# Performance work log

Hardware: AMD Instinct MI355X
Metric: run time of the kernel (lower is better)

The kernel has to match this reference:

```python
import jax, jax.numpy as jnp
import numpy as np

B = 8192      # batch_size
D = 1024      # d_model
E = 8         # num_domains
OUT = 2       # binary fake/real logits


def setup_inputs() -> dict:
    key = jax.random.key(0)
    k_feat, k_ids, k_w1, k_b1, k_w2, k_b2 = jax.random.split(key, 6)
    feature = jax.random.normal(k_feat, (B, D), dtype=jnp.float32)
    domain_ids = jax.random.randint(k_ids, (B,), 0, E, dtype=jnp.int64)
    # Per-domain expert parameters (torch Linear init ~ U(-1/sqrt(fan_in), 1/sqrt(fan_in)))
    s1 = 1.0 / np.sqrt(D)
    W1 = jax.random.uniform(k_w1, (E, D, D), jnp.float32, -s1, s1)   # acts as x @ W1[e]
    b1 = jax.random.uniform(k_b1, (E, D), jnp.float32, -s1, s1)
    W2 = jax.random.uniform(k_w2, (E, D, OUT), jnp.float32, -s1, s1)
    b2 = jax.random.uniform(k_b2, (E, OUT), jnp.float32, -s1, s1)
    return {"feature": feature, "domain_ids": domain_ids,
            "W1": W1, "b1": b1, "W2": W2, "b2": b2}


def reference(feature, domain_ids, W1, b1, W2, b2):
    # Eval-mode forward (Dropout is identity at inference).
    # Layer 1: compute for all E experts (E is small), then select per sample.
    # h_all: [B, E, D]
    h_all = jnp.einsum('bd,edh->beh', feature, W1)
    sel = jnp.arange(feature.shape[0])
    h = h_all[sel, domain_ids] + b1[domain_ids]          # [B, D]
    h = jax.nn.relu(h)
    # Layer 2: gather the tiny [D, 2] head per sample.
    logits = jnp.einsum('bd,bdo->bo', h, W2[domain_ids]) + b2[domain_ids]  # [B, 2]
    return logits
```

## Files before the change

### kernel.cpp

```cpp
#include <hip/hip_runtime.h>
#include <hip/hip_bf16.h>

#define NB 8192
#define ND 1024
#define NE 8

typedef unsigned short u16;
typedef __bf16 bf16x8 __attribute__((ext_vector_type(8)));
typedef float f32x4 __attribute__((ext_vector_type(4)));
typedef u16 u16x8 __attribute__((ext_vector_type(8)));
typedef u16 u16x2 __attribute__((ext_vector_type(2)));

__device__ __forceinline__ u16 f2bf(float f) {
    union { float f; unsigned u; } v; v.f = f;
    unsigned r = v.u + 0x7fffu + ((v.u >> 16) & 1u);
    return (u16)(r >> 16);
}

__global__ __launch_bounds__(1024) void k_prep(const int* __restrict__ ids,
    const float* __restrict__ b2, float* __restrict__ out,
    int* __restrict__ counts, int* __restrict__ offs, int* __restrict__ bucket)
{
    __shared__ int s_cnt[NE], s_off[NE];
    int t = threadIdx.x;
    if (t < NE) s_cnt[t] = 0;
    __syncthreads();
    #pragma unroll
    for (int i = 0; i < NB / 1024; ++i) {
        int b = t + i * 1024;
        int e = ids[b];
        atomicAdd(&s_cnt[e], 1);
        out[2 * b]     = b2[2 * e];
        out[2 * b + 1] = b2[2 * e + 1];
    }
    __syncthreads();
    if (t == 0) {
        int acc = 0;
        #pragma unroll
        for (int e2 = 0; e2 < NE; ++e2) {
            counts[e2] = s_cnt[e2];
            offs[e2] = acc;
            s_off[e2] = acc;
            acc += s_cnt[e2];
        }
    }
    __syncthreads();
    #pragma unroll
    for (int i = 0; i < NB / 1024; ++i) {
        int b = t + i * 1024;
        int e = ids[b];
        int pos = atomicAdd(&s_off[e], 1);
        bucket[pos] = b;
    }
}

__global__ __launch_bounds__(256) void k_cvt(const float* __restrict__ X, u16* __restrict__ Xb,
                                             const float* __restrict__ W1, u16* __restrict__ W1t)
{
    __shared__ float s[64][65];
    int bid = blockIdx.x;
    int t = threadIdx.x;
    if (bid < 4096) {
        long i = ((long)bid * 256 + t) * 8;
        f32x4 a = *(const f32x4*)(X + i);
        f32x4 b = *(const f32x4*)(X + i + 4);
        u16x8 o;
        o[0] = f2bf(a[0]); o[1] = f2bf(a[1]); o[2] = f2bf(a[2]); o[3] = f2bf(a[3]);
        o[4] = f2bf(b[0]); o[5] = f2bf(b[1]); o[6] = f2bf(b[2]); o[7] = f2bf(b[3]);
        *(u16x8*)(Xb + i) = o;
        return;
    }
    int bid2 = bid - 4096;
    int e = bid2 >> 8;
    int tr = ((bid2 >> 4) & 15) << 6;
    int tc = (bid2 & 15) << 6;
    const float* src = W1 + (size_t)e * ND * ND;
    u16* dst = W1t + (size_t)e * ND * ND;
    #pragma unroll
    for (int i = 0; i < 4; ++i) {
        int idx = i * 256 + t;
        int r = idx >> 4, c4 = (idx & 15) * 4;
        f32x4 v = *(const f32x4*)(src + (size_t)(tr + r) * ND + tc + c4);
        s[c4 + 0][r] = v[0]; s[c4 + 1][r] = v[1];
        s[c4 + 2][r] = v[2]; s[c4 + 3][r] = v[3];
    }
    __syncthreads();
    #pragma unroll
    for (int i = 0; i < 8; ++i) {
        int chunk = i * 256 + t;
        int n = chunk >> 5, k = (chunk & 31) * 2;
        u16x2 o;
        o[0] = f2bf(s[n][k]);
        o[1] = f2bf(s[n][k + 1]);
        *(u16x2*)(dst + (size_t)(tc + n) * ND + tr + k) = o;
    }
}

#define GLDS16(src, dst) __builtin_amdgcn_global_load_lds( \
    (const __attribute__((address_space(1))) void*)(src), \
    (__attribute__((address_space(3))) void*)(dst), 16, 0, 0)

__global__ __launch_bounds__(256) void k_gemm(
    const u16* __restrict__ Xb, const u16* __restrict__ W1t,
    const float* __restrict__ b1, const float* __restrict__ W2,
    const int* __restrict__ counts, const int* __restrict__ offs,
    const int* __restrict__ bucket, float* __restrict__ out)
{
    __shared__ u16 sA[4][4096];
    __shared__ u16 sB[4][4096];
    __shared__ int sRows[128];

    int bid = blockIdx.x;
    int e  = bid & 7;
    int nt = (bid >> 3) & 7;
    int mt = bid >> 6;

    int cnt = counts[e];
    if (mt * 128 >= cnt) return;
    int off = offs[e];
    int rem = cnt - mt * 128;

    int t = threadIdx.x;
    if (t < 128) {
        int r = mt * 128 + t;
        sRows[t] = bucket[off + (r < cnt ? r : 0)];
    }
    __syncthreads();

    int n0 = nt * 128;
    int c0 = t, c1 = t + 256;
    int ar0 = c0 >> 2, as0 = (c0 & 3) * 8;
    int ar1 = c1 >> 2, as1 = (c1 & 3) * 8;
    const u16* a0p = Xb + (size_t)sRows[ar0] * ND + as0;
    const u16* a1p = Xb + (size_t)sRows[ar1] * ND + as1;
    const u16* b0p = W1t + ((size_t)e * ND + n0 + ar0) * ND + as0;
    const u16* b1p = W1t + ((size_t)e * ND + n0 + ar1) * ND + as1;
    int w = t >> 6;
    int l = t & 63;
    int lc = l & 15, kg = l >> 4;
    int wm = (w >> 1) * 64, wn = (w & 1) * 64;

    f32x4 acc[4][4] = {};

    char* sA0 = (char*)sA;
    char* sB0 = (char*)sB;

    auto stage = [&](int buf, int kt) {
        int k0 = kt * 32;
        GLDS16(a0p + k0, sA0 + buf * 8192 + w * 1024);
        GLDS16(a1p + k0, sA0 + buf * 8192 + 4096 + w * 1024);
        GLDS16(b0p + k0, sB0 + buf * 8192 + w * 1024);
        GLDS16(b1p + k0, sB0 + buf * 8192 + 4096 + w * 1024);
    };
    auto compute = [&](int buf) {
        const char* Ab = sA0 + buf * 8192;
        const char* Bb = sB0 + buf * 8192;
        bf16x8 af[4], bfr[4];
        #pragma unroll
        for (int mf = 0; mf < 4; ++mf)
            af[mf] = *(const bf16x8*)(Ab + (wm + mf * 16 + lc) * 64 + kg * 16);
        #pragma unroll
        for (int nf = 0; nf < 4; ++nf)
            bfr[nf] = *(const bf16x8*)(Bb + (wn + nf * 16 + lc) * 64 + kg * 16);
        #pragma unroll
        for (int mf = 0; mf < 4; ++mf) {
            #pragma unroll
            for (int nf = 0; nf < 4; ++nf)
                acc[mf][nf] = __builtin_amdgcn_mfma_f32_16x16x32_bf16(af[mf], bfr[nf], acc[mf][nf], 0, 0, 0);
        }
    };

    stage(0, 0); stage(1, 1); stage(2, 2);

    #pragma unroll 4
    for (int kt = 0; kt < 32; ++kt) {
        if (kt < 30)      asm volatile("s_waitcnt vmcnt(8)" ::: "memory");
        else if (kt == 30) asm volatile("s_waitcnt vmcnt(4)" ::: "memory");
        else               asm volatile("s_waitcnt vmcnt(0)" ::: "memory");
        asm volatile("s_barrier" ::: "memory");
        if (kt < 29) stage((kt + 3) & 3, kt + 3);
        compute(kt & 3);
    }

    float b1v[4], w20[4], w21[4];
    #pragma unroll
    for (int nf = 0; nf < 4; ++nf) {
        int ncol = n0 + wn + nf * 16 + lc;
        b1v[nf] = b1[e * ND + ncol];
        w20[nf] = W2[((size_t)e * ND + ncol) * 2 + 0];
        w21[nf] = W2[((size_t)e * ND + ncol) * 2 + 1];
    }
    #pragma unroll
    for (int mf = 0; mf < 4; ++mf) {
        #pragma unroll
        for (int r = 0; r < 4; ++r) {
            float s0 = 0.f, s1 = 0.f;
            #pragma unroll
            for (int nf = 0; nf < 4; ++nf) {
                float h = acc[mf][nf][r] + b1v[nf];
                h = fmaxf(h, 0.f);
                s0 += h * w20[nf];
                s1 += h * w21[nf];
            }
            #pragma unroll
            for (int m = 8; m >= 1; m >>= 1) {
                s0 += __shfl_xor(s0, m, 64);
                s1 += __shfl_xor(s1, m, 64);
            }
            int row = wm + mf * 16 + kg * 4 + r;
            if (lc == 0 && row < rem) {
                int b = sRows[row];
                atomicAdd(&out[2 * b], s0);
                atomicAdd(&out[2 * b + 1], s1);
            }
        }
    }
}

extern "C" void kernel_launch(void* const* d_in, const int* in_sizes, int n_in,
                              void* d_out, int out_size, void* d_ws, size_t ws_size,
                              hipStream_t stream)
{
    const float* X   = (const float*)d_in[0];
    const int*   ids = (const int*)d_in[1];
    const float* W1  = (const float*)d_in[2];
    const float* b1  = (const float*)d_in[3];
    const float* W2  = (const float*)d_in[4];
    const float* b2  = (const float*)d_in[5];
    float* out = (float*)d_out;

    char* ws = (char*)d_ws;
    int* counts = (int*)ws;
    int* offs   = (int*)(ws + 32);
    int* bucket = (int*)(ws + 64);
    u16* Xb     = (u16*)(ws + 65536);
    u16* W1t    = (u16*)(ws + 65536 + (size_t)NB * ND * 2);

    k_prep<<<1, 1024, 0, stream>>>(ids, b2, out, counts, offs, bucket);
    k_cvt<<<4096 + 2048, 256, 0, stream>>>(X, Xb, W1, W1t);
    k_gemm<<<16 * 64, 256, 0, stream>>>(Xb, W1t, b1, W2, counts, offs, bucket, out);
}
```

Before: 172.3 us.

## Fold bucketing into the convert kernel and shrink GEMM tiles to 64x128

The single-block prep kernel is replaced by extra blocks in the conversion kernel. Those blocks bucket samples per expert with wave ballots and one atomic per wave, writing into fixed-stride buckets, and a memset clears the counts first. The GEMM tile drops from 128x128 with a 4-stage LDS pipeline to 64x128 with double buffering, which doubles the block count so the CUs are better filled. Each block now reuses less data and the pipeline is shallower. The W1 transpose store is also widened to 4-element vectors.

Measured after the change: 176.1 us. 2.2% more time.

```diff
diff --git a/kernel.cpp b/kernel.cpp
--- a/kernel.cpp
+++ b/kernel.cpp
@@ -4,12 +4,13 @@
 #define NB 8192
 #define ND 1024
 #define NE 8
+#define BSTRIDE 2048
 
 typedef unsigned short u16;
 typedef __bf16 bf16x8 __attribute__((ext_vector_type(8)));
 typedef float f32x4 __attribute__((ext_vector_type(4)));
 typedef u16 u16x8 __attribute__((ext_vector_type(8)));
-typedef u16 u16x2 __attribute__((ext_vector_type(2)));
+typedef u16 u16x4 __attribute__((ext_vector_type(4)));
 
 __device__ __forceinline__ u16 f2bf(float f) {
     union { float f; unsigned u; } v; v.f = f;
@@ -17,47 +18,12 @@
     return (u16)(r >> 16);
 }
 
-__global__ __launch_bounds__(1024) void k_prep(const int* __restrict__ ids,
-    const float* __restrict__ b2, float* __restrict__ out,
-    int* __restrict__ counts, int* __restrict__ offs, int* __restrict__ bucket)
+__global__ __launch_bounds__(256) void k_pre(
+    const float* __restrict__ X, u16* __restrict__ Xb,
+    const float* __restrict__ W1, u16* __restrict__ W1t,
+    const int* __restrict__ ids, const float* __restrict__ b2,
+    float* __restrict__ out, int* __restrict__ counts, int* __restrict__ bucket)
 {
-    __shared__ int s_cnt[NE], s_off[NE];
-    int t = threadIdx.x;
-    if (t < NE) s_cnt[t] = 0;
-    __syncthreads();
-    #pragma unroll
-    for (int i = 0; i < NB / 1024; ++i) {
-        int b = t + i * 1024;
-        int e = ids[b];
-        atomicAdd(&s_cnt[e], 1);
-        out[2 * b]     = b2[2 * e];
-        out[2 * b + 1] = b2[2 * e + 1];
-    }
-    __syncthreads();
-    if (t == 0) {
-        int acc = 0;
-        #pragma unroll
-        for (int e2 = 0; e2 < NE; ++e2) {
-            counts[e2] = s_cnt[e2];
-            offs[e2] = acc;
-            s_off[e2] = acc;
-            acc += s_cnt[e2];
-        }
-    }
-    __syncthreads();
-    #pragma unroll
-    for (int i = 0; i < NB / 1024; ++i) {
-        int b = t + i * 1024;
-        int e = ids[b];
-        int pos = atomicAdd(&s_off[e], 1);
-        bucket[pos] = b;
-    }
-}
-
-__global__ __launch_bounds__(256) void k_cvt(const float* __restrict__ X, u16* __restrict__ Xb,
-                                             const float* __restrict__ W1, u16* __restrict__ W1t)
-{
-    __shared__ float s[64][65];
     int bid = blockIdx.x;
     int t = threadIdx.x;
     if (bid < 4096) {
@@ -70,30 +36,54 @@
         *(u16x8*)(Xb + i) = o;
         return;
     }
-    int bid2 = bid - 4096;
-    int e = bid2 >> 8;
-    int tr = ((bid2 >> 4) & 15) << 6;
-    int tc = (bid2 & 15) << 6;
-    const float* src = W1 + (size_t)e * ND * ND;
-    u16* dst = W1t + (size_t)e * ND * ND;
+    if (bid < 6144) {
+        __shared__ float s[64][65];
+        int bid2 = bid - 4096;
+        int e = bid2 >> 8;
+        int tr = ((bid2 >> 4) & 15) << 6;
+        int tc = (bid2 & 15) << 6;
+        const float* src = W1 + (size_t)e * ND * ND;
+        u16* dst = W1t + (size_t)e * ND * ND;
+        #pragma unroll
+        for (int i = 0; i < 4; ++i) {
+            int idx = i * 256 + t;
+            int r = idx >> 4, c4 = (idx & 15) * 4;
+            f32x4 v = *(const f32x4*)(src + (size_t)(tr + r) * ND + tc + c4);
+            s[c4 + 0][r] = v[0]; s[c4 + 1][r] = v[1];
+            s[c4 + 2][r] = v[2]; s[c4 + 3][r] = v[3];
+        }
+        __syncthreads();
+        #pragma unroll
+        for (int i = 0; i < 4; ++i) {
+            int idx = i * 256 + t;
+            int n = idx >> 4, k4 = (idx & 15) * 4;
+            u16x4 o;
+            o[0] = f2bf(s[n][k4 + 0]); o[1] = f2bf(s[n][k4 + 1]);
+            o[2] = f2bf(s[n][k4 + 2]); o[3] = f2bf(s[n][k4 + 3]);
+            *(u16x4*)(dst + (size_t)(tc + n) * ND + tr + k4) = o;
+        }
+        return;
+    }
+    int b = (bid - 6144) * 256 + t;
+    int e = ids[b];
+    out[2 * b]     = b2[2 * e];
+    out[2 * b + 1] = b2[2 * e + 1];
+    int lane = t & 63;
+    unsigned long long lt = (1ull << lane) - 1ull;
+    int pos = 0;
     #pragma unroll
-    for (int i = 0; i < 4; ++i) {
-        int idx = i * 256 + t;
-        int r = idx >> 4, c4 = (idx & 15) * 4;
-        f32x4 v = *(const f32x4*)(src + (size_t)(tr + r) * ND + tc + c4);
-        s[c4 + 0][r] = v[0]; s[c4 + 1][r] = v[1];
-        s[c4 + 2][r] = v[2]; s[c4 + 3][r] = v[3];
-    }
-    __syncthreads();
-    #pragma unroll
-    for (int i = 0; i < 8; ++i) {
-        int chunk = i * 256 + t;
-        int n = chunk >> 5, k = (chunk & 31) * 2;
-        u16x2 o;
-        o[0] = f2bf(s[n][k]);
-        o[1] = f2bf(s[n][k + 1]);
-        *(u16x2*)(dst + (size_t)(tc + n) * ND + tr + k) = o;
-    }
+    for (int ee = 0; ee < NE; ++ee) {
+        unsigned long long m = __ballot(e == ee);
+        if (m) {
+            int leader = __ffsll((long long)m) - 1;
+            int r = __popcll(m & lt);
+            int base = 0;
+            if (e == ee && r == 0) base = atomicAdd(&counts[ee], __popcll(m));
+            base = __shfl(base, leader, 64);
+            if (e == ee) pos = base + r;
+        }
+    }
+    bucket[e * BSTRIDE + pos] = b;
 }
 
 #define GLDS16(src, dst) __builtin_amdgcn_global_load_lds( \
@@ -103,12 +93,12 @@
 __global__ __launch_bounds__(256) void k_gemm(
     const u16* __restrict__ Xb, const u16* __restrict__ W1t,
     const float* __restrict__ b1, const float* __restrict__ W2,
-    const int* __restrict__ counts, const int* __restrict__ offs,
-    const int* __restrict__ bucket, float* __restrict__ out)
+    const int* __restrict__ counts, const int* __restrict__ bucket,
+    float* __restrict__ out)
 {
-    __shared__ u16 sA[4][4096];
-    __shared__ u16 sB[4][4096];
-    __shared__ int sRows[128];
+    __shared__ u16 sA[2][2048];
+    __shared__ u16 sB[2][4096];
+    __shared__ int sRows[64];
 
     int bid = blockIdx.x;
     int e  = bid & 7;
@@ -116,70 +106,67 @@
     int mt = bid >> 6;
 
     int cnt = counts[e];
-    if (mt * 128 >= cnt) return;
-    int off = offs[e];
-    int rem = cnt - mt * 128;
+    if (mt * 64 >= cnt) return;
+    int rem = cnt - mt * 64;
 
     int t = threadIdx.x;
-    if (t < 128) {
-        int r = mt * 128 + t;
-        sRows[t] = bucket[off + (r < cnt ? r : 0)];
+    if (t < 64) {
+        int r = mt * 64 + t;
+        sRows[t] = bucket[e * BSTRIDE + (r < cnt ? r : 0)];
     }
     __syncthreads();
 
     int n0 = nt * 128;
-    int c0 = t, c1 = t + 256;
-    int ar0 = c0 >> 2, as0 = (c0 & 3) * 8;
-    int ar1 = c1 >> 2, as1 = (c1 & 3) * 8;
-    const u16* a0p = Xb + (size_t)sRows[ar0] * ND + as0;
-    const u16* a1p = Xb + (size_t)sRows[ar1] * ND + as1;
-    const u16* b0p = W1t + ((size_t)e * ND + n0 + ar0) * ND + as0;
-    const u16* b1p = W1t + ((size_t)e * ND + n0 + ar1) * ND + as1;
+    int ar = t >> 2, as = (t & 3) * 8;
+    const u16* ap  = Xb + (size_t)sRows[ar] * ND + as;
+    const u16* b0p = W1t + ((size_t)e * ND + n0 + ar) * ND + as;
+    const u16* b1p = W1t + ((size_t)e * ND + n0 + 64 + ar) * ND + as;
     int w = t >> 6;
     int l = t & 63;
     int lc = l & 15, kg = l >> 4;
-    int wm = (w >> 1) * 64, wn = (w & 1) * 64;
-
-    f32x4 acc[4][4] = {};
-
-    char* sA0 = (char*)sA;
-    char* sB0 = (char*)sB;
+    int wm = (w >> 1) * 32, wn = (w & 1) * 64;
+
+    f32x4 acc[2][4] = {};
+
+    char* A0 = (char*)sA;
+    char* B0 = (char*)sB;
 
     auto stage = [&](int buf, int kt) {
         int k0 = kt * 32;
-        GLDS16(a0p + k0, sA0 + buf * 8192 + w * 1024);
-        GLDS16(a1p + k0, sA0 + buf * 8192 + 4096 + w * 1024);
-        GLDS16(b0p + k0, sB0 + buf * 8192 + w * 1024);
-        GLDS16(b1p + k0, sB0 + buf * 8192 + 4096 + w * 1024);
+        GLDS16(ap  + k0, A0 + buf * 4096 + w * 1024);
+        GLDS16(b0p + k0, B0 + buf * 8192 + w * 1024);
+        GLDS16(b1p + k0, B0 + buf * 8192 + 4096 + w * 1024);
     };
-    auto compute = [&](int buf) {
-        const char* Ab = sA0 + buf * 8192;
-        const char* Bb = sB0 + buf * 8192;
-        bf16x8 af[4], bfr[4];
-        #pragma unroll
-        for (int mf = 0; mf < 4; ++mf)
+
+    stage(0, 0);
+
+    #pragma unroll 2
+    for (int kt = 0; kt < 32; ++kt) {
+        int buf = kt & 1;
+        if (kt + 1 < 32) {
+            stage(buf ^ 1, kt + 1);
+            asm volatile("s_waitcnt vmcnt(3)" ::: "memory");
+        } else {
+            asm volatile("s_waitcnt vmcnt(0)" ::: "memory");
+        }
+        asm volatile("s_barrier" ::: "memory");
+
+        const char* Ab = A0 + buf * 4096;
+        const char* Bb = B0 + buf * 8192;
+        bf16x8 af[2], bfr[4];
+        #pragma unroll
+        for (int mf = 0; mf < 2; ++mf)
             af[mf] = *(const bf16x8*)(Ab + (wm + mf * 16 + lc) * 64 + kg * 16);
         #pragma unroll
         for (int nf = 0; nf < 4; ++nf)
             bfr[nf] = *(const bf16x8*)(Bb + (wn + nf * 16 + lc) * 64 + kg * 16);
         #pragma unroll
-        for (int mf = 0; mf < 4; ++mf) {
+        for (int mf = 0; mf < 2; ++mf) {
             #pragma unroll
             for (int nf = 0; nf < 4; ++nf)
                 acc[mf][nf] = __builtin_amdgcn_mfma_f32_16x16x32_bf16(af[mf], bfr[nf], acc[mf][nf], 0, 0, 0);
         }
-    };
-
-    stage(0, 0); stage(1, 1); stage(2, 2);
-
-    #pragma unroll 4
-    for (int kt = 0; kt < 32; ++kt) {
-        if (kt < 30)      asm volatile("s_waitcnt vmcnt(8)" ::: "memory");
-        else if (kt == 30) asm volatile("s_waitcnt vmcnt(4)" ::: "memory");
-        else               asm volatile("s_waitcnt vmcnt(0)" ::: "memory");
         asm volatile("s_barrier" ::: "memory");
-        if (kt < 29) stage((kt + 3) & 3, kt + 3);
-        compute(kt & 3);
     }
 
     float b1v[4], w20[4], w21[4];
@@ -191,7 +178,7 @@
         w21[nf] = W2[((size_t)e * ND + ncol) * 2 + 1];
     }
     #pragma unroll
-    for (int mf = 0; mf < 4; ++mf) {
+    for (int mf = 0; mf < 2; ++mf) {
         #pragma unroll
         for (int r = 0; r < 4; ++r) {
             float s0 = 0.f, s1 = 0.f;
@@ -231,12 +218,11 @@
 
     char* ws = (char*)d_ws;
     int* counts = (int*)ws;
-    int* offs   = (int*)(ws + 32);
-    int* bucket = (int*)(ws + 64);
-    u16* Xb     = (u16*)(ws + 65536);
-    u16* W1t    = (u16*)(ws + 65536 + (size_t)NB * ND * 2);
-
-    k_prep<<<1, 1024, 0, stream>>>(ids, b2, out, counts, offs, bucket);
-    k_cvt<<<4096 + 2048, 256, 0, stream>>>(X, Xb, W1, W1t);
-    k_gemm<<<16 * 64, 256, 0, stream>>>(Xb, W1t, b1, W2, counts, offs, bucket, out);
-}
+    int* bucket = (int*)(ws + 4096);
+    u16* Xb     = (u16*)(ws + 131072);
+    u16* W1t    = (u16*)(ws + 131072 + (size_t)NB * ND * 2);
+
+    hipMemsetAsync(counts, 0, NE * sizeof(int), stream);
+    k_pre<<<4096 + 2048 + 32, 256, 0, stream>>>(X, Xb, W1, W1t, ids, b2, out, counts, bucket);
+    k_gemm<<<32 * 64, 256, 0, stream>>>(Xb, W1t, b1, W2, counts, bucket, out);
+}
```
